# Optimization experiments

Hardware: AMD Instinct MI355X
Metric: run time of the kernel (lower is better)

Reference implementation:

```python
import jax, jax.numpy as jnp
import numpy as np

# irreps config: (multiplicity, l) for "128x0e + 64x1o + 32x2e" (in == out)
IRREPS = [(128, 0), (64, 1), (32, 2)]


def setup_inputs() -> dict:
    key = jax.random.key(0)
    k0, k1, k2, k3 = jax.random.split(key, 4)
    N = 200000
    dim = sum(mul * (2 * l + 1) for mul, l in IRREPS)  # 480
    x = jax.random.normal(k0, (N, dim), dtype=jnp.float32)
    W0 = jax.random.normal(k1, (128, 128), dtype=jnp.float32)
    W1 = jax.random.normal(k2, (64, 64), dtype=jnp.float32)
    W2 = jax.random.normal(k3, (32, 32), dtype=jnp.float32)
    return {"x": x, "W0": W0, "W1": W1, "W2": W2}


def _irrep_linear(x, weights):
    # x: [N, dim_in]; per-irrep: reshape block to [N, mul, 2l+1], contract mul dim,
    # scale by 1/sqrt(fan_in) = 1/sqrt(mul_in) (e3nn default path normalization).
    outs = []
    off = 0
    for (mul, l), W in zip(IRREPS, weights):
        d = 2 * l + 1
        blk = x[:, off:off + mul * d].reshape(-1, mul, d)  # [N, mul, d]
        alpha = 1.0 / np.sqrt(mul)
        y = jnp.einsum('nid,io->nod', blk, W) * jnp.float32(alpha)  # [N, mul_out, d]
        outs.append(y.reshape(-1, mul * d))
        off += mul * d
    return jnp.concatenate(outs, axis=-1)  # [N, dim_out]


def reference(x, W0, W1, W2):
    return _irrep_linear(x, (W0, W1, W2))
```

## Files before the change

kernel.cpp:

```cpp
#include <hip/hip_runtime.h>

typedef _Float16 v8h __attribute__((ext_vector_type(8)));
typedef float    v4f __attribute__((ext_vector_type(4)));

#define MFMA16(a, b, c) __builtin_amdgcn_mfma_f32_16x16x32_f16((a), (b), (c), 0, 0, 0)

#define GLL16(gptr, lptr)                                                        \
  __builtin_amdgcn_global_load_lds((const __attribute__((address_space(1))) void*)(gptr), \
                                   (__attribute__((address_space(3))) void*)(lptr), 16, 0, 0)


__global__ void build_frags_k(const float* __restrict__ W0, const float* __restrict__ W1,
                              const float* __restrict__ W2, v8h* __restrict__ frag) {
  const int f = blockIdx.x;
  const int lane = threadIdx.x;
  int ot, kt;
  if (f < 32)       { ot = f >> 2;           kt = f & 3; }
  else if (f < 104) { int q = f - 32;  ot = 8 + q / 6;  kt = 4 + q % 6; }
  else              { int q = f - 104; ot = 20 + q / 5; kt = 10 + q % 5; }
  const int n  = ot * 16 + (lane & 15);
  const int kb = kt * 32 + (lane >> 4) * 8;
  v8h v;
#pragma unroll
  for (int e = 0; e < 8; ++e) {
    const int k = kb + e;
    float wv = 0.0f;
    if (k < 128) {
      if (n < 128) wv = W0[k * 128 + n] * 0.08838834764831845f;
    } else if (k < 320) {
      if (n >= 128 && n < 320) {
        const int i = k - 128, o = n - 128;
        if (i % 3 == o % 3) wv = W1[(i / 3) * 64 + (o / 3)] * 0.125f;
      }
    } else {
      if (n >= 320) {
        const int i = k - 320, o = n - 320;
        if (i % 5 == o % 5) wv = W2[(i / 5) * 32 + (o / 5)] * 0.17677669529663687f;
      }
    }
    v[e] = (_Float16)wv;
  }
  frag[f * 64 + lane] = v;
}

template <int V>
__device__ __forceinline__ void wave_main(const float* __restrict__ x,
                                          const v8h* __restrict__ frag,
                                          float* __restrict__ out,
                                          unsigned char* sm, int t, int t0, int t1) {
  const int lane = t & 63;
  const int w    = t >> 6;
  const int r16  = lane & 15;
  const int g    = lane >> 4;

  constexpr int NF = (V == 0) ? 21 : (V == 1) ? 20 : 15;
  v8h f[NF];
  {
    const int fb0 = w * 4;
    const int fb1 = 32 + w * 6;
#pragma unroll
    for (int k = 0; k < 4; ++k) f[k] = frag[(fb0 + k) * 64 + lane];
#pragma unroll
    for (int k = 0; k < 6; ++k) f[4 + k] = frag[(fb1 + k) * 64 + lane];
    if constexpr (V == 0) {
      const int fb2 = 32 + (8 + w) * 6;
      const int fb3 = 104 + (4 + w) * 5;
#pragma unroll
      for (int k = 0; k < 6; ++k) f[10 + k] = frag[(fb2 + k) * 64 + lane];
#pragma unroll
      for (int k = 0; k < 5; ++k) f[16 + k] = frag[(fb3 + k) * 64 + lane];
    } else if constexpr (V == 1) {
      const int fb2 = 104 + (w - 4) * 5;
      const int fb3 = 104 + (w + 4) * 5;
#pragma unroll
      for (int k = 0; k < 5; ++k) f[10 + k] = frag[(fb2 + k) * 64 + lane];
#pragma unroll
      for (int k = 0; k < 5; ++k) f[15 + k] = frag[(fb3 + k) * 64 + lane];
    } else {
      const int fb2 = 104 + (w - 4) * 5;
#pragma unroll
      for (int k = 0; k < 5; ++k) f[10 + k] = frag[(fb2 + k) * 64 + lane];
    }
  }

  auto stage = [&](int tt, int bsel) {
    const unsigned char* xt = (const unsigned char*)x + (size_t)tt * 61440u;
    unsigned char* buf = sm + bsel * 61440;
#pragma unroll
    for (int i = 0; i < 8; ++i) {
      if (i < 7 || t < 256) {
        const unsigned gl = (unsigned)(i * 512 + t);
        const unsigned r  = gl / 120u;
        const unsigned j  = gl - r * 120u;
        GLL16(xt + r * 1920u + ((j ^ (r & 7u)) << 4), buf + i * 8192 + w * 1024);
      }
    }
  };

#define LDAF(kt, dst)                                                                       \
  {                                                                                         \
    const unsigned j0 = (unsigned)((kt) * 8 + g * 2);                                       \
    const float4 lo = *reinterpret_cast<const float4*>(smc + rb + (((j0) ^ q) << 4));       \
    const float4 hi = *reinterpret_cast<const float4*>(smc + rb + ((((j0) + 1) ^ q) << 4)); \
    v8h v_;                                                                                 \
    v_[0] = (_Float16)lo.x; v_[1] = (_Float16)lo.y;                                         \
    v_[2] = (_Float16)lo.z; v_[3] = (_Float16)lo.w;                                         \
    v_[4] = (_Float16)hi.x; v_[5] = (_Float16)hi.y;                                         \
    v_[6] = (_Float16)hi.z; v_[7] = (_Float16)hi.w;                                         \
    dst = v_;                                                                               \
  }

  auto compute = [&](int tt, int bsel) {
    const unsigned char* smc = sm + bsel * 61440;
#pragma unroll
    for (int sl = 0; sl < 2; ++sl) {
      const unsigned row = (unsigned)(sl * 16 + r16);
      const unsigned rb  = row * 1920u;
      const unsigned q   = row & 7u;
      float* const ob = out + ((size_t)tt * 32 + sl * 16 + r16) * 480 + g * 4;
      {
        v8h x0[4];
#pragma unroll
        for (int k = 0; k < 4; ++k) LDAF(k, x0[k]);
        v4f a0 = {0.f, 0.f, 0.f, 0.f};
#pragma unroll
        for (int k = 0; k < 4; ++k) a0 = MFMA16(f[k], x0[k], a0);
        *reinterpret_cast<v4f*>(ob + w * 16) = a0;
      }
      {
        v8h x1[6];
#pragma unroll
        for (int k = 0; k < 6; ++k) LDAF(4 + k, x1[k]);
        v4f a1 = {0.f, 0.f, 0.f, 0.f};
#pragma unroll
        for (int k = 0; k < 6; ++k) a1 = MFMA16(f[4 + k], x1[k], a1);
        *reinterpret_cast<v4f*>(ob + (8 + w) * 16) = a1;
        if constexpr (V == 0) {
          v4f a2 = {0.f, 0.f, 0.f, 0.f};
#pragma unroll
          for (int k = 0; k < 6; ++k) a2 = MFMA16(f[10 + k], x1[k], a2);
          *reinterpret_cast<v4f*>(ob + (16 + w) * 16) = a2;
        }
      }
      {
        v8h x2[5];
#pragma unroll
        for (int k = 0; k < 5; ++k) LDAF(10 + k, x2[k]);
        if constexpr (V == 0) {
          v4f a3 = {0.f, 0.f, 0.f, 0.f};
#pragma unroll
          for (int k = 0; k < 5; ++k) a3 = MFMA16(f[16 + k], x2[k], a3);
          *reinterpret_cast<v4f*>(ob + (24 + w) * 16) = a3;
        } else if constexpr (V == 1) {
          v4f a2 = {0.f, 0.f, 0.f, 0.f}, a3 = {0.f, 0.f, 0.f, 0.f};
#pragma unroll
          for (int k = 0; k < 5; ++k) {
            a2 = MFMA16(f[10 + k], x2[k], a2);
            a3 = MFMA16(f[15 + k], x2[k], a3);
          }
          *reinterpret_cast<v4f*>(ob + (16 + w) * 16) = a2;
          *reinterpret_cast<v4f*>(ob + (24 + w) * 16) = a3;
        } else {
          v4f a2 = {0.f, 0.f, 0.f, 0.f};
#pragma unroll
          for (int k = 0; k < 5; ++k) a2 = MFMA16(f[10 + k], x2[k], a2);
          *reinterpret_cast<v4f*>(ob + (16 + w) * 16) = a2;
        }
      }
    }
  };

  stage(t0, 0);
  int tt = t0;
  for (; tt < t1 - 1; ++tt) {
    const int cur = (tt - t0) & 1;
    stage(tt + 1, cur ^ 1);
    if constexpr (V == 0) asm volatile("s_waitcnt vmcnt(8)" ::: "memory");
    else                  asm volatile("s_waitcnt vmcnt(7)" ::: "memory");
    __builtin_amdgcn_s_barrier();
    compute(tt, cur);
    __builtin_amdgcn_s_barrier();
  }
  {
    const int cur = (tt - t0) & 1;
    asm volatile("s_waitcnt vmcnt(0)" ::: "memory");
    __builtin_amdgcn_s_barrier();
    compute(tt, cur);
  }
#undef LDAF
}

__global__ __launch_bounds__(512, 2) void irrep_linear_k(
    const float* __restrict__ x, const v8h* __restrict__ frag, float* __restrict__ out,
    int base_tpb, int rem) {
  __shared__ __align__(16) unsigned char sm[2 * 61440];
  const int t = threadIdx.x;
  const int b = blockIdx.x;
  const int t0 = b * base_tpb + (b < rem ? b : rem);
  const int t1 = t0 + base_tpb + (b < rem ? 1 : 0);
  const int w = t >> 6;
  if (w < 4)      wave_main<0>(x, frag, out, sm, t, t0, t1);
  else if (w < 6) wave_main<1>(x, frag, out, sm, t, t0, t1);
  else            wave_main<2>(x, frag, out, sm, t, t0, t1);
}

extern "C" void kernel_launch(void* const* d_in, const int* in_sizes, int n_in,
                              void* d_out, int out_size, void* d_ws, size_t ws_size,
                              hipStream_t stream) {
  const float* x  = (const float*)d_in[0];
  const float* W0 = (const float*)d_in[1];
  const float* W1 = (const float*)d_in[2];
  const float* W2 = (const float*)d_in[3];
  float* out = (float*)d_out;
  v8h* frag = (v8h*)d_ws;

  build_frags_k<<<154, 64, 0, stream>>>(W0, W1, W2, frag);

  const int N = in_sizes[0] / 480;
  const int n_tiles = N / 32;
  const int nblk = 256;
  const int base_tpb = n_tiles / nblk;
  const int rem = n_tiles - base_tpb * nblk;
  irrep_linear_k<<<nblk, 512, 0, stream>>>(x, frag, out, base_tpb, rem);
}
```

Baseline: 177.7 us.

## Switch to 16-row tiles with a four-slot LDS ring and three-deep prefetch

Halves the row tile from 32 to 16 and replaces the double-buffered LDS staging with a four-slot ring buffer of the same total size. Global-to-LDS loads now run three tiles ahead, with explicit prologue and epilogue stages. The vmcnt waits are derived from per-wave load and store counts so each wave only waits for its oldest tile. The aim is to keep more bytes in flight and hide HBM latency better in this memory-bound kernel. The cost is twice as many barrier pairs per row, since each tile now covers half as many rows.

```diff
diff --git a/kernel.cpp b/kernel.cpp
--- a/kernel.cpp
+++ b/kernel.cpp
@@ -53,6 +53,9 @@
   const int r16  = lane & 15;
   const int g    = lane >> 4;
 
+  constexpr int G = (V == 2) ? 3 : 4;
+  constexpr int S = (V == 2) ? 3 : 4;
+
   constexpr int NF = (V == 0) ? 21 : (V == 1) ? 20 : 15;
   v8h f[NF];
   {
@@ -83,12 +86,12 @@
     }
   }
 
-  auto stage = [&](int tt, int bsel) {
-    const unsigned char* xt = (const unsigned char*)x + (size_t)tt * 61440u;
-    unsigned char* buf = sm + bsel * 61440;
-#pragma unroll
-    for (int i = 0; i < 8; ++i) {
-      if (i < 7 || t < 256) {
+  auto stage = [&](int tt) {
+    const unsigned char* xt = (const unsigned char*)x + (size_t)tt * 30720u;
+    unsigned char* buf = sm + (size_t)(tt & 3) * 30720u;
+#pragma unroll
+    for (int i = 0; i < 4; ++i) {
+      if (i < 3 || w < 6) {
         const unsigned gl = (unsigned)(i * 512 + t);
         const unsigned r  = gl / 120u;
         const unsigned j  = gl - r * 120u;
@@ -110,90 +113,89 @@
     dst = v_;                                                                               \
   }
 
-  auto compute = [&](int tt, int bsel) {
-    const unsigned char* smc = sm + bsel * 61440;
-#pragma unroll
-    for (int sl = 0; sl < 2; ++sl) {
-      const unsigned row = (unsigned)(sl * 16 + r16);
-      const unsigned rb  = row * 1920u;
-      const unsigned q   = row & 7u;
-      float* const ob = out + ((size_t)tt * 32 + sl * 16 + r16) * 480 + g * 4;
-      {
-        v8h x0[4];
-#pragma unroll
-        for (int k = 0; k < 4; ++k) LDAF(k, x0[k]);
-        v4f a0 = {0.f, 0.f, 0.f, 0.f};
-#pragma unroll
-        for (int k = 0; k < 4; ++k) a0 = MFMA16(f[k], x0[k], a0);
-        *reinterpret_cast<v4f*>(ob + w * 16) = a0;
-      }
-      {
-        v8h x1[6];
-#pragma unroll
-        for (int k = 0; k < 6; ++k) LDAF(4 + k, x1[k]);
-        v4f a1 = {0.f, 0.f, 0.f, 0.f};
-#pragma unroll
-        for (int k = 0; k < 6; ++k) a1 = MFMA16(f[4 + k], x1[k], a1);
-        *reinterpret_cast<v4f*>(ob + (8 + w) * 16) = a1;
-        if constexpr (V == 0) {
-          v4f a2 = {0.f, 0.f, 0.f, 0.f};
-#pragma unroll
-          for (int k = 0; k < 6; ++k) a2 = MFMA16(f[10 + k], x1[k], a2);
-          *reinterpret_cast<v4f*>(ob + (16 + w) * 16) = a2;
+  auto compute = [&](int tt) {
+    const unsigned char* smc = sm + (size_t)(tt & 3) * 30720u;
+    const unsigned rb = (unsigned)r16 * 1920u;
+    const unsigned q  = (unsigned)(r16 & 7u);
+    float* const ob = out + ((size_t)tt * 16 + r16) * 480 + g * 4;
+    {
+      v8h x0[4];
+#pragma unroll
+      for (int k = 0; k < 4; ++k) LDAF(k, x0[k]);
+      v4f a0 = {0.f, 0.f, 0.f, 0.f};
+#pragma unroll
+      for (int k = 0; k < 4; ++k) a0 = MFMA16(f[k], x0[k], a0);
+      *reinterpret_cast<v4f*>(ob + w * 16) = a0;
+    }
+    {
+      v8h x1[6];
+#pragma unroll
+      for (int k = 0; k < 6; ++k) LDAF(4 + k, x1[k]);
+      v4f a1 = {0.f, 0.f, 0.f, 0.f};
+#pragma unroll
+      for (int k = 0; k < 6; ++k) a1 = MFMA16(f[4 + k], x1[k], a1);
+      *reinterpret_cast<v4f*>(ob + (8 + w) * 16) = a1;
+      if constexpr (V == 0) {
+        v4f a2 = {0.f, 0.f, 0.f, 0.f};
+#pragma unroll
+        for (int k = 0; k < 6; ++k) a2 = MFMA16(f[10 + k], x1[k], a2);
+        *reinterpret_cast<v4f*>(ob + (16 + w) * 16) = a2;
+      }
+    }
+    {
+      v8h x2[5];
+#pragma unroll
+      for (int k = 0; k < 5; ++k) LDAF(10 + k, x2[k]);
+      if constexpr (V == 0) {
+        v4f a3 = {0.f, 0.f, 0.f, 0.f};
+#pragma unroll
+        for (int k = 0; k < 5; ++k) a3 = MFMA16(f[16 + k], x2[k], a3);
+        *reinterpret_cast<v4f*>(ob + (24 + w) * 16) = a3;
+      } else if constexpr (V == 1) {
+        v4f a2 = {0.f, 0.f, 0.f, 0.f}, a3 = {0.f, 0.f, 0.f, 0.f};
+#pragma unroll
+        for (int k = 0; k < 5; ++k) {
+          a2 = MFMA16(f[10 + k], x2[k], a2);
+          a3 = MFMA16(f[15 + k], x2[k], a3);
         }
-      }
-      {
-        v8h x2[5];
-#pragma unroll
-        for (int k = 0; k < 5; ++k) LDAF(10 + k, x2[k]);
-        if constexpr (V == 0) {
-          v4f a3 = {0.f, 0.f, 0.f, 0.f};
-#pragma unroll
-          for (int k = 0; k < 5; ++k) a3 = MFMA16(f[16 + k], x2[k], a3);
-          *reinterpret_cast<v4f*>(ob + (24 + w) * 16) = a3;
-        } else if constexpr (V == 1) {
-          v4f a2 = {0.f, 0.f, 0.f, 0.f}, a3 = {0.f, 0.f, 0.f, 0.f};
-#pragma unroll
-          for (int k = 0; k < 5; ++k) {
-            a2 = MFMA16(f[10 + k], x2[k], a2);
-            a3 = MFMA16(f[15 + k], x2[k], a3);
-          }
-          *reinterpret_cast<v4f*>(ob + (16 + w) * 16) = a2;
-          *reinterpret_cast<v4f*>(ob + (24 + w) * 16) = a3;
-        } else {
-          v4f a2 = {0.f, 0.f, 0.f, 0.f};
-#pragma unroll
-          for (int k = 0; k < 5; ++k) a2 = MFMA16(f[10 + k], x2[k], a2);
-          *reinterpret_cast<v4f*>(ob + (16 + w) * 16) = a2;
-        }
+        *reinterpret_cast<v4f*>(ob + (16 + w) * 16) = a2;
+        *reinterpret_cast<v4f*>(ob + (24 + w) * 16) = a3;
+      } else {
+        v4f a2 = {0.f, 0.f, 0.f, 0.f};
+#pragma unroll
+        for (int k = 0; k < 5; ++k) a2 = MFMA16(f[10 + k], x2[k], a2);
+        *reinterpret_cast<v4f*>(ob + (16 + w) * 16) = a2;
       }
     }
   };
 
-  stage(t0, 0);
-  int tt = t0;
-  for (; tt < t1 - 1; ++tt) {
-    const int cur = (tt - t0) & 1;
-    stage(tt + 1, cur ^ 1);
-    if constexpr (V == 0) asm volatile("s_waitcnt vmcnt(8)" ::: "memory");
-    else                  asm volatile("s_waitcnt vmcnt(7)" ::: "memory");
-    __builtin_amdgcn_s_barrier();
-    compute(tt, cur);
-    __builtin_amdgcn_s_barrier();
-  }
-  {
-    const int cur = (tt - t0) & 1;
-    asm volatile("s_waitcnt vmcnt(0)" ::: "memory");
-    __builtin_amdgcn_s_barrier();
-    compute(tt, cur);
-  }
+#define PIPE_ITER(TT, N)                                        \
+  {                                                             \
+    asm volatile("s_waitcnt vmcnt(%0)" :: "n"(N) : "memory");   \
+    __builtin_amdgcn_s_barrier();                               \
+    compute(TT);                                                \
+    __builtin_amdgcn_s_barrier();                               \
+  }
+
+  stage(t0); stage(t0 + 1); stage(t0 + 2);
+  stage(t0 + 3); PIPE_ITER(t0,     3 * G)
+  stage(t0 + 4); PIPE_ITER(t0 + 1, 3 * G + S)
+  stage(t0 + 5); PIPE_ITER(t0 + 2, 3 * G + 2 * S)
+  for (int tt = t0 + 3; tt < t1 - 3; ++tt) {
+    stage(tt + 3);
+    PIPE_ITER(tt, 3 * G + 3 * S)
+  }
+  for (int tt = t1 - 3; tt < t1; ++tt) {
+    PIPE_ITER(tt, S)
+  }
+#undef PIPE_ITER
 #undef LDAF
 }
 
 __global__ __launch_bounds__(512, 2) void irrep_linear_k(
     const float* __restrict__ x, const v8h* __restrict__ frag, float* __restrict__ out,
     int base_tpb, int rem) {
-  __shared__ __align__(16) unsigned char sm[2 * 61440];
+  __shared__ __align__(16) unsigned char sm[4 * 30720];
   const int t = threadIdx.x;
   const int b = blockIdx.x;
   const int t0 = b * base_tpb + (b < rem ? b : rem);
@@ -217,7 +219,7 @@
   build_frags_k<<<154, 64, 0, stream>>>(W0, W1, W2, frag);
 
   const int N = in_sizes[0] / 480;
-  const int n_tiles = N / 32;
+  const int n_tiles = N / 16;
   const int nblk = 256;
   const int base_tpb = n_tiles / nblk;
   const int rem = n_tiles - base_tpb * nblk;
```

Result: slower. 206.8 us (+16.4%).
